# Performance work log

Measured on AMD Instinct MI355X. Metric: run time of the kernel, lower is better.

Reference implementation:

```python
import jax, jax.numpy as jnp
import numpy as np

I, T, L, E, H, W = 256, 256, 32, 128, 7, 7

def setup_inputs() -> dict:
    key = jax.random.key(0)
    k1, k2, k3 = jax.random.split(key, 3)
    image_features = jax.random.normal(k1, (I, E, H, W), dtype=jnp.float32)
    text_features = jax.random.normal(k2, (T, L, E), dtype=jnp.float32)
    text_length = jax.random.randint(k3, (T,), 1, L + 1, dtype=jnp.int32)
    logit_neg_log_temperature = jnp.asarray(-np.log(0.07), dtype=jnp.float32)
    return {
        "image_features": image_features,
        "text_features": text_features,
        "text_length": text_length,
        "logit_neg_log_temperature": logit_neg_log_temperature,
    }

def reference(image_features, text_features, text_length, logit_neg_log_temperature):
    # image_features: [I, E, H, W]; text_features: [T, L, E]
    i, e, h, w = image_features.shape
    img = image_features.reshape(i, e, h * w)            # [I, E, HW]
    # cross-modal similarity per (image, text, token, patch): [I, T, L, HW]
    sim = jnp.einsum('iep,tle->itlp', img, text_features)
    # max over patches, then sum over tokens, normalized by caption length
    match_max = jnp.max(sim, axis=3)                     # [I, T, L]
    match = jnp.sum(match_max, axis=2) / text_length.astype(match_max.dtype)  # [I, T]
    logit_scale = jnp.exp(logit_neg_log_temperature)
    logits_per_image = match * logit_scale
    logits_per_text = match.T * logit_scale
    return (logits_per_image, logits_per_text)
```

## Files before the change

### kernel.cpp

```cpp
#include <hip/hip_runtime.h>
#include <hip/hip_bf16.h>

typedef __attribute__((ext_vector_type(8))) short bf16x8;
typedef __attribute__((ext_vector_type(4))) float f32x4;

#define I_N 256
#define T_N 256
#define L_N 32
#define E_N 128
#define P_N 49
#define TG  4

__global__ __launch_bounds__(256) void pack_all(const float* __restrict__ txt,
                                                const float* __restrict__ img,
                                                unsigned short* __restrict__ bpre,
                                                unsigned short* __restrict__ apre) {
    const int bid = blockIdx.x;
    if (bid < 512) {
        int gid  = bid * 256 + threadIdx.x;
        int lane = gid & 63;
        int kk   = (gid >> 6) & 3;
        int tt   = gid >> 8;
        int row  = tt * 16 + (lane & 15);
        int e0   = kk * 32 + (lane >> 4) * 8;
        const float* src = txt + row * E_N + e0;
        union { unsigned short u[8]; bf16x8 v; } o;
        #pragma unroll
        for (int j = 0; j < 8; ++j) {
            __hip_bfloat16 h = __float2bfloat16(src[j]);
            o.u[j] = *reinterpret_cast<unsigned short*>(&h);
        }
        ((bf16x8*)bpre)[gid] = o.v;
    } else {
        int gid   = (bid - 512) * 256 + threadIdx.x;
        int lane  = gid & 63;
        int kk    = (gid >> 6) & 3;
        int pt    = (gid >> 8) & 3;
        int i     = gid >> 10;
        int patch = pt * 16 + (lane & 15);
        int e0    = kk * 32 + (lane >> 4) * 8;
        const float* src = img + i * (E_N * P_N) + e0 * P_N + patch;
        union { unsigned short u[8]; bf16x8 v; } o;
        #pragma unroll
        for (int j = 0; j < 8; ++j) {
            float x = (patch < P_N) ? src[j * P_N] : 0.0f;
            __hip_bfloat16 h = __float2bfloat16(x);
            o.u[j] = *reinterpret_cast<unsigned short*>(&h);
        }
        ((bf16x8*)apre)[gid] = o.v;
    }
}

__global__ __launch_bounds__(512) void clip_mfma(
    const unsigned short* __restrict__ apre,
    const unsigned short* __restrict__ bpre,
    const int*   __restrict__ tlen,
    const float* __restrict__ nlt,
    float*       __restrict__ out) {

    __shared__ short sB[2][TG * 8 * 512];

    const int wid  = threadIdx.x >> 6;
    const int lane = threadIdx.x & 63;
    const int i    = blockIdx.y * 8 + wid;
    const int t0   = blockIdx.x * 16;
    const float scale = expf(nlt[0]);
    const bool  lo16  = (lane < 16);

    bf16x8 af[4][4];
    const bf16x8* ap = (const bf16x8*)apre + (size_t)i * 16 * 64;
    #pragma unroll
    for (int pt = 0; pt < 4; ++pt)
        #pragma unroll
        for (int kk = 0; kk < 4; ++kk)
            af[pt][kk] = ap[(pt * 4 + kk) * 64 + lane];

    auto stage = [&](int buf, int g) {
        #pragma unroll
        for (int q = 0; q < 4; ++q) {
            int fl = wid * 4 + q;
            int t  = t0 + g * TG + (fl >> 3);
            int f  = fl & 7;
            const unsigned short* src = bpre + ((size_t)(t * 8 + f)) * 512 + lane * 8;
            short* dst = &sB[buf][fl * 512];
            __builtin_amdgcn_global_load_lds(
                (const __attribute__((address_space(1))) unsigned int*)(const void*)src,
                (__attribute__((address_space(3))) unsigned int*)(void*)dst, 16, 0, 0);
        }
    };

    auto reduceT = [&](f32x4 (&a)[4][2], int t) {
        float colmax[2];
        #pragma unroll
        for (int ctt = 0; ctt < 2; ++ctt) {
            float m[4];
            #pragma unroll
            for (int r = 0; r < 4; ++r)
                m[r] = fmaxf(fmaxf(a[0][ctt][r], a[1][ctt][r]), a[2][ctt][r]);
            m[0] = fmaxf(m[0], lo16 ? a[3][ctt][0] : -INFINITY);
            float mm = fmaxf(fmaxf(m[0], m[1]), fmaxf(m[2], m[3]));
            mm = fmaxf(mm, __shfl_xor(mm, 16));
            mm = fmaxf(mm, __shfl_xor(mm, 32));
            colmax[ctt] = mm;
        }
        float s = colmax[0] + colmax[1];
        #pragma unroll
        for (int off = 1; off <= 8; off <<= 1)
            s += __shfl_xor(s, off);
        if (lane == 0) {
            float match = (s / (float)tlen[t]) * scale;
            out[i * T_N + t]             = match;
            out[I_N * T_N + t * I_N + i] = match;
        }
    };

    bf16x8 bf[2][2][4];
    f32x4  acc[2][4][2];

    stage(0, 0);
    __syncthreads();

    #pragma unroll
    for (int tx = 0; tx < 16; ++tx) {
        const int p   = tx & 1;
        const int gg  = tx >> 2;
        const int txg = tx & 3;

        if ((tx & 3) == 0) {
            if (tx > 0) __syncthreads();
            if (gg + 1 < 4) stage((gg + 1) & 1, gg + 1);
        }

        const bf16x8* bfp = (const bf16x8*)&sB[gg & 1][0];
        #pragma unroll
        for (int ctt = 0; ctt < 2; ++ctt)
            #pragma unroll
            for (int kk = 0; kk < 4; ++kk)
                bf[p][ctt][kk] = bfp[(txg * 8 + ctt * 4 + kk) * 64 + lane];

        #pragma unroll
        for (int pt = 0; pt < 4; ++pt)
            #pragma unroll
            for (int ctt = 0; ctt < 2; ++ctt)
                acc[p][pt][ctt] = (f32x4){0.f, 0.f, 0.f, 0.f};

        #pragma unroll
        for (int kk = 0; kk < 4; ++kk)
            #pragma unroll
            for (int pt = 0; pt < 4; ++pt)
                #pragma unroll
                for (int ctt = 0; ctt < 2; ++ctt)
                    acc[p][pt][ctt] = __builtin_amdgcn_mfma_f32_16x16x32_bf16(
                        af[pt][kk], bf[p][ctt][kk], acc[p][pt][ctt], 0, 0, 0);

        if (tx > 0) reduceT(acc[1 - p], t0 + tx - 1);
    }
    reduceT(acc[1], t0 + 15);
}

extern "C" void kernel_launch(void* const* d_in, const int* in_sizes, int n_in,
                              void* d_out, int out_size, void* d_ws, size_t ws_size,
                              hipStream_t stream) {
    const float* img  = (const float*)d_in[0];
    const float* txt  = (const float*)d_in[1];
    const int*   tlen = (const int*)d_in[2];
    const float* nlt  = (const float*)d_in[3];
    float*       out  = (float*)d_out;

    unsigned short* bpre = (unsigned short*)d_ws;
    unsigned short* apre = (unsigned short*)((char*)d_ws + (2u << 20));

    pack_all<<<1536, 256, 0, stream>>>(txt, img, bpre, apre);

    dim3 grid(16, 32);
    clip_mfma<<<grid, 512, 0, stream>>>(apre, bpre, tlen, nlt, out);
}
```

Baseline: 45.54 us.

## Switch to 32x32x16 bf16 MFMA with repacked operands and 4-wave blocks

Replaces the 16x16x32 MFMA tiling with 32x32x16 instructions so one MFMA covers all 32 tokens and 32 patches. The pack kernel changes its layout to match, the max/sum reduction is rewritten for the 16-element accumulator layout, and blocks shrink to 4 waves with twice as many blocks along the image axis. The aim is fewer MFMA issues and fewer cross-lane shuffles per text item. The cost is more wasted patch padding (64 padded vs 49 real) and a different register and occupancy profile.

```diff
diff --git a/kernel.cpp b/kernel.cpp
--- a/kernel.cpp
+++ b/kernel.cpp
@@ -1,8 +1,8 @@
 #include <hip/hip_runtime.h>
 #include <hip/hip_bf16.h>
 
-typedef __attribute__((ext_vector_type(8))) short bf16x8;
-typedef __attribute__((ext_vector_type(4))) float f32x4;
+typedef __attribute__((ext_vector_type(8)))  short bf16x8;
+typedef __attribute__((ext_vector_type(16))) float f32x16;
 
 #define I_N 256
 #define T_N 256
@@ -19,11 +19,11 @@
     if (bid < 512) {
         int gid  = bid * 256 + threadIdx.x;
         int lane = gid & 63;
-        int kk   = (gid >> 6) & 3;
-        int tt   = gid >> 8;
-        int row  = tt * 16 + (lane & 15);
-        int e0   = kk * 32 + (lane >> 4) * 8;
-        const float* src = txt + row * E_N + e0;
+        int ks   = (gid >> 6) & 7;
+        int t    = gid >> 9;
+        int l    = lane & 31;
+        int e0   = ks * 16 + (lane >> 5) * 8;
+        const float* src = txt + (t * L_N + l) * E_N + e0;
         union { unsigned short u[8]; bf16x8 v; } o;
         #pragma unroll
         for (int j = 0; j < 8; ++j) {
@@ -34,11 +34,11 @@
     } else {
         int gid   = (bid - 512) * 256 + threadIdx.x;
         int lane  = gid & 63;
-        int kk    = (gid >> 6) & 3;
-        int pt    = (gid >> 8) & 3;
+        int ks    = (gid >> 6) & 7;
+        int pt    = (gid >> 9) & 1;
         int i     = gid >> 10;
-        int patch = pt * 16 + (lane & 15);
-        int e0    = kk * 32 + (lane >> 4) * 8;
+        int patch = pt * 32 + (lane & 31);
+        int e0    = ks * 16 + (lane >> 5) * 8;
         const float* src = img + i * (E_N * P_N) + e0 * P_N + patch;
         union { unsigned short u[8]; bf16x8 v; } o;
         #pragma unroll
@@ -51,7 +51,7 @@
     }
 }
 
-__global__ __launch_bounds__(512) void clip_mfma(
+__global__ __launch_bounds__(256) void clip_mfma(
     const unsigned short* __restrict__ apre,
     const unsigned short* __restrict__ bpre,
     const int*   __restrict__ tlen,
@@ -62,23 +62,23 @@
 
     const int wid  = threadIdx.x >> 6;
     const int lane = threadIdx.x & 63;
-    const int i    = blockIdx.y * 8 + wid;
+    const int i    = blockIdx.y * 4 + wid;
     const int t0   = blockIdx.x * 16;
     const float scale = expf(nlt[0]);
-    const bool  lo16  = (lane < 16);
+    const bool  lo32  = (lane < 32);
 
-    bf16x8 af[4][4];
+    bf16x8 af[2][8];
     const bf16x8* ap = (const bf16x8*)apre + (size_t)i * 16 * 64;
     #pragma unroll
-    for (int pt = 0; pt < 4; ++pt)
+    for (int pt = 0; pt < 2; ++pt)
         #pragma unroll
-        for (int kk = 0; kk < 4; ++kk)
-            af[pt][kk] = ap[(pt * 4 + kk) * 64 + lane];
+        for (int ks = 0; ks < 8; ++ks)
+            af[pt][ks] = ap[(pt * 8 + ks) * 64 + lane];
 
     auto stage = [&](int buf, int g) {
         #pragma unroll
-        for (int q = 0; q < 4; ++q) {
-            int fl = wid * 4 + q;
+        for (int q = 0; q < 8; ++q) {
+            int fl = wid * 8 + q;
             int t  = t0 + g * TG + (fl >> 3);
             int f  = fl & 7;
             const unsigned short* src = bpre + ((size_t)(t * 8 + f)) * 512 + lane * 8;
@@ -89,23 +89,17 @@
         }
     };
 
-    auto reduceT = [&](f32x4 (&a)[4][2], int t) {
-        float colmax[2];
+    auto reduceT = [&](f32x16 (&a)[2], int t) {
+        float m = a[0][0];
         #pragma unroll
-        for (int ctt = 0; ctt < 2; ++ctt) {
-            float m[4];
-            #pragma unroll
-            for (int r = 0; r < 4; ++r)
-                m[r] = fmaxf(fmaxf(a[0][ctt][r], a[1][ctt][r]), a[2][ctt][r]);
-            m[0] = fmaxf(m[0], lo16 ? a[3][ctt][0] : -INFINITY);
-            float mm = fmaxf(fmaxf(m[0], m[1]), fmaxf(m[2], m[3]));
-            mm = fmaxf(mm, __shfl_xor(mm, 16));
-            mm = fmaxf(mm, __shfl_xor(mm, 32));
-            colmax[ctt] = mm;
-        }
-        float s = colmax[0] + colmax[1];
+        for (int r = 1; r < 16; ++r) m = fmaxf(m, a[0][r]);
         #pragma unroll
-        for (int off = 1; off <= 8; off <<= 1)
+        for (int r = 0; r < 8; ++r)  m = fmaxf(m, a[1][r]);
+        m = fmaxf(m, lo32 ? a[1][8] : -INFINITY);
+        m = fmaxf(m, __shfl_xor(m, 32));
+        float s = m;
+        #pragma unroll
+        for (int off = 1; off <= 16; off <<= 1)
             s += __shfl_xor(s, off);
         if (lane == 0) {
             float match = (s / (float)tlen[t]) * scale;
@@ -114,8 +108,8 @@
         }
     };
 
-    bf16x8 bf[2][2][4];
-    f32x4  acc[2][4][2];
+    bf16x8 bf[2][8];
+    f32x16 acc[2][2];
 
     stage(0, 0);
     __syncthreads();
@@ -133,25 +127,21 @@
 
         const bf16x8* bfp = (const bf16x8*)&sB[gg & 1][0];
         #pragma unroll
-        for (int ctt = 0; ctt < 2; ++ctt)
-            #pragma unroll
-            for (int kk = 0; kk < 4; ++kk)
-                bf[p][ctt][kk] = bfp[(txg * 8 + ctt * 4 + kk) * 64 + lane];
+        for (int ks = 0; ks < 8; ++ks)
+            bf[p][ks] = bfp[(txg * 8 + ks) * 64 + lane];
 
         #pragma unroll
-        for (int pt = 0; pt < 4; ++pt)
+        for (int pt = 0; pt < 2; ++pt)
             #pragma unroll
-            for (int ctt = 0; ctt < 2; ++ctt)
-                acc[p][pt][ctt] = (f32x4){0.f, 0.f, 0.f, 0.f};
+            for (int r = 0; r < 16; ++r)
+                acc[p][pt][r] = 0.0f;
 
         #pragma unroll
-        for (int kk = 0; kk < 4; ++kk)
+        for (int ks = 0; ks < 8; ++ks)
             #pragma unroll
-            for (int pt = 0; pt < 4; ++pt)
-                #pragma unroll
-                for (int ctt = 0; ctt < 2; ++ctt)
-                    acc[p][pt][ctt] = __builtin_amdgcn_mfma_f32_16x16x32_bf16(
-                        af[pt][kk], bf[p][ctt][kk], acc[p][pt][ctt], 0, 0, 0);
+            for (int pt = 0; pt < 2; ++pt)
+                acc[p][pt] = __builtin_amdgcn_mfma_f32_32x32x16_bf16(
+                    af[pt][ks], bf[p][ks], acc[p][pt], 0, 0, 0);
 
         if (tx > 0) reduceT(acc[1 - p], t0 + tx - 1);
     }
@@ -172,6 +162,6 @@
 
     pack_all<<<1536, 256, 0, stream>>>(txt, img, bpre, apre);
 
-    dim3 grid(16, 32);
-    clip_mfma<<<grid, 512, 0, stream>>>(apre, bpre, tlen, nlt, out);
+    dim3 grid(16, 64);
+    clip_mfma<<<grid, 256, 0, stream>>>(apre, bpre, tlen, nlt, out);
 }
```

Measured after the change: 45.13 us. About the same (-0.9%).
